# Optimization experiments

Measured on AMD Instinct MI355X. Metric: run time of the kernel, lower is better.

The kernel has to match this reference:

```python
import jax, jax.numpy as jnp
import numpy as np

B, CZ, E, V, H, W = 256, 512, 512, 4096, 16, 16  # batch, z_channels, embed_dim, vocab, latent HxW


def setup_inputs() -> dict:
    key = jax.random.key(0)
    k0, k1, k2, k3 = jax.random.split(key, 4)
    x = jax.random.normal(k0, (B, CZ, H, W), jnp.float32)          # encoder feature map
    pre_w = jax.random.normal(k1, (E, CZ), jnp.float32) * 0.02     # 1x1 pre_quant_conv weight
    pre_b = jnp.zeros((E,), jnp.float32)
    emb = jax.random.uniform(k2, (V, E), jnp.float32, -1.0 / V, 1.0 / V)  # codebook, uniform init as in module
    post_w = jax.random.normal(k3, (CZ, E), jnp.float32) * 0.02    # 1x1 post_quant_conv weight
    post_b = jnp.zeros((CZ,), jnp.float32)
    return dict(x=x, pre_w=pre_w, pre_b=pre_b, emb=emb, post_w=post_w, post_b=post_b)


def reference(x, pre_w, pre_b, emb, post_w, post_b):
    # pre_quant_conv: 1x1 Conv2d(CZ -> E)
    z = jnp.einsum('bchw,ec->behw', x, pre_w) + pre_b[None, :, None, None]
    b, e, h, w = z.shape
    # flatten spatial: (b h w, e)
    zf = z.transpose(0, 2, 3, 1).reshape(-1, e)
    # expanded squared-distance to codebook: ||z||^2 + ||c||^2 - 2 z.c
    dist = (jnp.sum(zf * zf, axis=1, keepdims=True)
            + jnp.sum(emb * emb, axis=1)
            - 2.0 * zf @ emb.T)                                    # [bhw, V]
    tokens = jnp.argmin(dist, axis=-1)                             # [bhw] int
    z_q = emb[tokens].reshape(b, h, w, e).transpose(0, 3, 1, 2)    # gather -> [b,e,h,w]
    # straight-through estimator
    dec_in = z + jax.lax.stop_gradient(z_q - z)
    # post_quant_conv: 1x1 Conv2d(E -> CZ)
    rec = jnp.einsum('behw,ce->bchw', dec_in, post_w) + post_b[None, :, None, None]
    return z, z_q, rec
```

## Files before the change

kernel.cpp:

```cpp
#include <hip/hip_runtime.h>
#include <hip/hip_bf16.h>

typedef unsigned short u16;
typedef unsigned int   u32;
typedef unsigned long long u64;

using short8 = __attribute__((ext_vector_type(8))) short;
using f32x4  = __attribute__((ext_vector_type(4))) float;
using u16x8  = __attribute__((ext_vector_type(8))) unsigned short;

#define AS_GLOBAL __attribute__((address_space(1)))
#define AS_LDS    __attribute__((address_space(3)))

__device__ __forceinline__ u16 f2b(float x){
  u32 u = __float_as_uint(x);
  u32 r = (u + 0x7FFFu + ((u >> 16) & 1u)) >> 16;
  return (u16)r;
}
__device__ __forceinline__ float b2f(u16 h){ return __uint_as_float(((u32)h) << 16); }

__device__ __forceinline__ void gload16(u16* l, const u16* g){
  __builtin_amdgcn_global_load_lds((const AS_GLOBAL u32*)g, (AS_LDS u32*)l, 16, 0, 0);
}

__device__ __forceinline__ u64 umin64(u64 a, u64 b){ return a < b ? a : b; }

__device__ __forceinline__ u64 shfl_xor_u64(u64 v, int m){
  u32 lo = __shfl_xor((u32)v, m, 64);
  u32 hi = __shfl_xor((u32)(v >> 32), m, 64);
  return ((u64)hi << 32) | lo;
}

__global__ void k_cvt(const float* __restrict__ w, u16* __restrict__ d, int n){
  int i = blockIdx.x * 256 + threadIdx.x;
  if (i < n) d[i] = f2b(w[i]);
}

__global__ void k_cnorm(const float* __restrict__ emb, float* __restrict__ cnorm){
  int v = blockIdx.x, lane = threadIdx.x;
  const float* r = emb + (size_t)v * 512;
  float s = 0.f;
  #pragma unroll
  for (int i = 0; i < 8; ++i){ float x = r[lane + i * 64]; s += x * x; }
  #pragma unroll
  for (int off = 32; off; off >>= 1) s += __shfl_down(s, off, 64);
  if (lane == 0) cnorm[v] = s;
}

__global__ void k_tcvt(const float* __restrict__ src, u16* __restrict__ d){
  __shared__ float t[64][65];
  const int bid = blockIdx.x;
  const int b  = bid >> 5;
  const int rb = (bid >> 2) & 7;
  const int cb = bid & 3;
  const float* s = src + ((size_t)b * 512 + (size_t)rb * 64) * 256 + cb * 64;
  const int tid = threadIdx.x;
  #pragma unroll
  for (int j = 0; j < 4; ++j){
    int fl = j * 256 + tid;
    int r = fl >> 4, c4 = (fl & 15) * 4;
    float4 v = *(const float4*)(s + (size_t)r * 256 + c4);
    t[r][c4 + 0] = v.x; t[r][c4 + 1] = v.y; t[r][c4 + 2] = v.z; t[r][c4 + 3] = v.w;
  }
  __syncthreads();
  u16* o = d + ((size_t)b * 256 + (size_t)cb * 64) * 512 + rb * 64;
  #pragma unroll
  for (int j = 0; j < 2; ++j){
    int fl = j * 256 + tid;
    int c = fl >> 3, r8 = (fl & 7) * 8;
    u16x8 hv;
    #pragma unroll
    for (int i = 0; i < 8; ++i) hv[i] = f2b(t[r8 + i][c]);
    *(u16x8*)(o + (size_t)c * 512 + r8) = hv;
  }
}

__global__ void k_zq(const u64* __restrict__ keys, const float* __restrict__ emb, float* __restrict__ zq){
  int sidx = blockIdx.x * 64 + threadIdx.x;
  int b = sidx >> 8, s = sidx & 255;
  int v = (int)(u32)keys[sidx];
  const float4* er = (const float4*)(emb + (size_t)v * 512);
  float* o = zq + (size_t)b * 512 * 256 + s;
  #pragma unroll 4
  for (int e4 = 0; e4 < 128; ++e4){
    float4 vv = er[e4];
    o[(size_t)(e4 * 4 + 0) * 256] = vv.x;
    o[(size_t)(e4 * 4 + 1) * 256] = vv.y;
    o[(size_t)(e4 * 4 + 2) * 256] = vv.z;
    o[(size_t)(e4 * 4 + 3) * 256] = vv.w;
  }
}

template<int MODE>
__global__ __launch_bounds__(256, 4) void k_gemm(
    const u16* __restrict__ Ah,
    const u16* __restrict__ Bh,
    const u64* __restrict__ gkeys,
    const float* __restrict__ bias,
    float* __restrict__ Cout,
    int M, int mtbits)
{
  constexpr int K = 512;
  __shared__ __align__(16) u16 sA[128 * 64];
  __shared__ __align__(16) u16 sB[128 * 64];

  const int tid  = threadIdx.x;
  const int lane = tid & 63;
  const int wid  = tid >> 6;
  const int wm = wid >> 1, wn = wid & 1;

  const int nwg = gridDim.x;
  const int chunk = nwg >> 3;
  const int pb = blockIdx.x;
  const int bid = (pb & 7) * chunk + (pb >> 3);

  const int mt = bid & ((1 << mtbits) - 1);
  const int nt = (bid >> mtbits) & 1;
  const int b  = bid >> (mtbits + 1);
  const int m0 = mt * 128;
  const int n0 = nt * 128;
  const int bbase = b * 256;

  const u16* ga[4];
  const u16* gb[4];
  int ldso[4];
  #pragma unroll
  for (int i = 0; i < 4; ++i){
    int e = i * 256 + tid;
    int r = e >> 3;
    int sl = (e & 7) ^ (r & 7);
    ldso[i] = e * 8;
    ga[i] = Ah + (size_t)(m0 + r) * K + sl * 8;
    size_t brow;
    if (MODE == 2) brow = (size_t)(u32)gkeys[bbase + n0 + r];
    else           brow = (size_t)(bbase + n0 + r);
    gb[i] = Bh + brow * K + sl * 8;
  }

  const f32x4 zero4 = {0.f, 0.f, 0.f, 0.f};
  f32x4 acc[4][4];
  #pragma unroll
  for (int i = 0; i < 4; ++i)
    #pragma unroll
    for (int j = 0; j < 4; ++j) acc[i][j] = zero4;

  int aoff[2][4], boff[2][4];
  #pragma unroll
  for (int ks = 0; ks < 2; ++ks)
    #pragma unroll
    for (int f = 0; f < 4; ++f){
      int rA = wm * 64 + f * 16 + (lane & 15);
      aoff[ks][f] = rA * 64 + (((ks * 4 + (lane >> 4)) ^ (rA & 7)) * 8);
      int rB = wn * 64 + f * 16 + (lane & 15);
      boff[ks][f] = rB * 64 + (((ks * 4 + (lane >> 4)) ^ (rB & 7)) * 8);
    }

  for (int kt = 0; kt < 8; ++kt){
    const int k0 = kt * 64;
    #pragma unroll
    for (int i = 0; i < 4; ++i){
      gload16(&sA[ldso[i]], ga[i] + k0);
      gload16(&sB[ldso[i]], gb[i] + k0);
    }
    __syncthreads();
    #pragma unroll
    for (int ks = 0; ks < 2; ++ks){
      short8 ah[4], bh[4];
      #pragma unroll
      for (int f = 0; f < 4; ++f){
        ah[f] = *(const short8*)&sA[aoff[ks][f]];
        bh[f] = *(const short8*)&sB[boff[ks][f]];
      }
      #pragma unroll
      for (int fm = 0; fm < 4; ++fm)
        #pragma unroll
        for (int fn = 0; fn < 4; ++fn)
          acc[fm][fn] = __builtin_amdgcn_mfma_f32_16x16x32_bf16(ah[fm], bh[fn], acc[fm][fn], 0, 0, 0);
    }
    __syncthreads();
  }

  const int row0 = m0 + wm * 64;
  const int col  = n0 + wn * 64 + (lane & 15);
  float* Cb = Cout + (size_t)b * M * 256;
  #pragma unroll
  for (int fm = 0; fm < 4; ++fm){
    #pragma unroll
    for (int j = 0; j < 4; ++j){
      int row = row0 + fm * 16 + (lane >> 4) * 4 + j;
      float bi = bias[row];
      #pragma unroll
      for (int fn = 0; fn < 4; ++fn)
        Cb[(size_t)row * 256 + col + fn * 16] = acc[fm][fn][j] + bi;
    }
  }
}

__global__ __launch_bounds__(512, 2) void k_gemm2(
    const u16* __restrict__ Ah,
    const u16* __restrict__ Bh,
    const float* __restrict__ cnorm,
    u64* __restrict__ okeys)
{
  __shared__ __align__(16) u16 lds[75776];

  const int tid  = threadIdx.x;
  const int lane = tid & 63;
  const int wid  = tid >> 6;
  const int wm   = wid >> 2;
  const int wn   = wid & 3;
  const int b    = blockIdx.x;
  const int bbase = b * 256;

  float* cn = (float*)&lds[65536];
  {
    const float4* c4 = (const float4*)cnorm;
    float4 a0 = c4[tid], a1 = c4[tid + 512];
    ((float4*)cn)[tid] = a0; ((float4*)cn)[tid + 512] = a1;
  }
  __syncthreads();

  const int l8 = lane >> 3;
  const int sl = (lane & 7) ^ l8;
  const int arb = (wid < 4) ? wid * 16 : 128 + (wid - 4) * 16;
  const int brb = (wid >> 1) * 64 + (wid & 1) * 16;
  const size_t aS = (size_t)(arb + l8) * 512 + sl * 8;
  const size_t bS = (size_t)(bbase + brb + l8) * 512 + sl * 8;
  const int dA = arb * 64 + lane * 8;
  const int dB = 16384 + brb * 64 + lane * 8;

#define STG_AFML(tp) if ((tp) < 128){ const u16* s_ = Ah + (size_t)((tp) >> 3) * 131072 + aS + ((tp) & 7) * 64; u16* d_ = &lds[((tp) & 1) * 32768 + dA]; gload16(d_, s_); gload16(d_ + 512, s_ + 4096); }
#define STG_AFMH(tp) if ((tp) < 128){ const u16* s_ = Ah + (size_t)((tp) >> 3) * 131072 + aS + 32768 + ((tp) & 7) * 64; u16* d_ = &lds[((tp) & 1) * 32768 + dA + 4096]; gload16(d_, s_); gload16(d_ + 512, s_ + 4096); }
#define STG_BFNL(tp) if ((tp) < 128){ const u16* s_ = Bh + bS + ((tp) & 7) * 64; u16* d_ = &lds[((tp) & 1) * 32768 + dB]; gload16(d_, s_); gload16(d_ + 512, s_ + 4096); }
#define STG_BFNH(tp) if ((tp) < 128){ const u16* s_ = Bh + bS + 16384 + ((tp) & 7) * 64; u16* d_ = &lds[((tp) & 1) * 32768 + dB + 2048]; gload16(d_, s_); gload16(d_ + 512, s_ + 4096); }

#define PH_WAIT(tau_) { if ((tau_) < 126){ asm volatile("s_waitcnt vmcnt(10)" ::: "memory"); } else { asm volatile("s_waitcnt vmcnt(0)" ::: "memory"); } \
  __builtin_amdgcn_s_barrier(); __builtin_amdgcn_sched_barrier(0); }

  int aoff[2][8], boff[2][4];
  #pragma unroll
  for (int ks = 0; ks < 2; ++ks){
    #pragma unroll
    for (int f = 0; f < 8; ++f){
      int rA = wm * 128 + f * 16 + (lane & 15);
      aoff[ks][f] = rA * 64 + (((ks * 4 + (lane >> 4)) ^ (rA & 7)) * 8);
    }
    #pragma unroll
    for (int f = 0; f < 4; ++f){
      int rB = wn * 64 + f * 16 + (lane & 15);
      boff[ks][f] = 16384 + rB * 64 + (((ks * 4 + (lane >> 4)) ^ (rB & 7)) * 8);
    }
  }

  const f32x4 zero4 = {0.f, 0.f, 0.f, 0.f};
  f32x4 acc[8][4];
  #pragma unroll
  for (int i = 0; i < 8; ++i)
    #pragma unroll
    for (int j = 0; j < 4; ++j) acc[i][j] = zero4;

  u64 best[4];
  #pragma unroll
  for (int i = 0; i < 4; ++i) best[i] = ~0ull;

  short8 ah[4][2], bhL[2][2], bhH[2][2];

  STG_AFML(0) STG_BFNL(0) STG_BFNH(0) STG_AFMH(0)
  STG_AFML(1) STG_BFNL(1) STG_BFNH(1)

  for (int mt = 0; mt < 16; ++mt){
    #pragma unroll 2
    for (int kt = 0; kt < 8; ++kt){
      const int tau = mt * 8 + kt;
      const int bb_ = (tau & 1) * 32768;

      PH_WAIT(tau);
      STG_AFMH(tau + 1)
      #pragma unroll
      for (int f = 0; f < 4; ++f){ ah[f][0] = *(const short8*)&lds[bb_ + aoff[0][f]]; ah[f][1] = *(const short8*)&lds[bb_ + aoff[1][f]]; }
      #pragma unroll
      for (int f = 0; f < 2; ++f){ bhL[f][0] = *(const short8*)&lds[bb_ + boff[0][f]]; bhL[f][1] = *(const short8*)&lds[bb_ + boff[1][f]]; }
      __builtin_amdgcn_s_setprio(1);
      #pragma unroll
      for (int fm = 0; fm < 4; ++fm)
        #pragma unroll
        for (int fn = 0; fn < 2; ++fn){
          acc[fm][fn] = __builtin_amdgcn_mfma_f32_16x16x32_bf16(ah[fm][0], bhL[fn][0], acc[fm][fn], 0, 0, 0);
          acc[fm][fn] = __builtin_amdgcn_mfma_f32_16x16x32_bf16(ah[fm][1], bhL[fn][1], acc[fm][fn], 0, 0, 0);
        }
      __builtin_amdgcn_s_setprio(0);
      __builtin_amdgcn_sched_barrier(0);

      PH_WAIT(tau);
      STG_AFML(tau + 2)
      #pragma unroll
      for (int f = 0; f < 2; ++f){ bhH[f][0] = *(const short8*)&lds[bb_ + boff[0][2 + f]]; bhH[f][1] = *(const short8*)&lds[bb_ + boff[1][2 + f]]; }
      __builtin_amdgcn_s_setprio(1);
      #pragma unroll
      for (int fm = 0; fm < 4; ++fm)
        #pragma unroll
        for (int fn = 0; fn < 2; ++fn){
          acc[fm][2 + fn] = __builtin_amdgcn_mfma_f32_16x16x32_bf16(ah[fm][0], bhH[fn][0], acc[fm][2 + fn], 0, 0, 0);
          acc[fm][2 + fn] = __builtin_amdgcn_mfma_f32_16x16x32_bf16(ah[fm][1], bhH[fn][1], acc[fm][2 + fn], 0, 0, 0);
        }
      __builtin_amdgcn_s_setprio(0);
      __builtin_amdgcn_sched_barrier(0);

      PH_WAIT(tau);
      STG_BFNL(tau + 2)
      #pragma unroll
      for (int f = 0; f < 4; ++f){ ah[f][0] = *(const short8*)&lds[bb_ + aoff[0][4 + f]]; ah[f][1] = *(const short8*)&lds[bb_ + aoff[1][4 + f]]; }
      __builtin_amdgcn_s_setprio(1);
      #pragma unroll
      for (int fm = 0; fm < 4; ++fm)
        #pragma unroll
        for (int fn = 0; fn < 2; ++fn){
          acc[4 + fm][2 + fn] = __builtin_amdgcn_mfma_f32_16x16x32_bf16(ah[fm][0], bhH[fn][0], acc[4 + fm][2 + fn], 0, 0, 0);
          acc[4 + fm][2 + fn] = __builtin_amdgcn_mfma_f32_16x16x32_bf16(ah[fm][1], bhH[fn][1], acc[4 + fm][2 + fn], 0, 0, 0);
        }
      __builtin_amdgcn_s_setprio(0);
      __builtin_amdgcn_sched_barrier(0);

      PH_WAIT(tau);
      STG_BFNH(tau + 2)
      __builtin_amdgcn_s_setprio(1);
      #pragma unroll
      for (int fm = 0; fm < 4; ++fm)
        #pragma unroll
        for (int fn = 0; fn < 2; ++fn){
          acc[4 + fm][fn] = __builtin_amdgcn_mfma_f32_16x16x32_bf16(ah[fm][0], bhL[fn][0], acc[4 + fm][fn], 0, 0, 0);
          acc[4 + fm][fn] = __builtin_amdgcn_mfma_f32_16x16x32_bf16(ah[fm][1], bhL[fn][1], acc[4 + fm][fn], 0, 0, 0);
        }
      __builtin_amdgcn_s_setprio(0);
      __builtin_amdgcn_sched_barrier(0);
    }

    #pragma unroll
    for (int fn = 0; fn < 4; ++fn){
      #pragma unroll
      for (int fm = 0; fm < 8; ++fm){
        #pragma unroll
        for (int j = 0; j < 4; ++j){
          int v = mt * 256 + wm * 128 + fm * 16 + (lane >> 4) * 4 + j;
          float sc = cn[v] - 2.0f * acc[fm][fn][j];
          u32 o = __float_as_uint(sc);
          o = (o & 0x80000000u) ? ~o : (o | 0x80000000u);
          best[fn] = umin64(best[fn], ((u64)o << 32) | (u32)v);
        }
      }
    }
    #pragma unroll
    for (int i = 0; i < 8; ++i)
      #pragma unroll
      for (int j = 0; j < 4; ++j) acc[i][j] = zero4;
  }

  #pragma unroll
  for (int fn = 0; fn < 4; ++fn){
    best[fn] = umin64(best[fn], shfl_xor_u64(best[fn], 16));
    best[fn] = umin64(best[fn], shfl_xor_u64(best[fn], 32));
  }
  u64* kbuf = (u64*)&lds[73728];
  __syncthreads();
  if (lane < 16){
    #pragma unroll
    for (int fn = 0; fn < 4; ++fn)
      kbuf[wm * 256 + wn * 64 + fn * 16 + lane] = best[fn];
  }
  __syncthreads();
  if (tid < 256)
    okeys[bbase + tid] = umin64(kbuf[tid], kbuf[256 + tid]);

#undef STG_AFML
#undef STG_AFMH
#undef STG_BFNL
#undef STG_BFNH
#undef PH_WAIT
}

extern "C" void kernel_launch(void* const* d_in, const int* in_sizes, int n_in,
                              void* d_out, int out_size, void* d_ws, size_t ws_size,
                              hipStream_t stream){
  const float* x      = (const float*)d_in[0];
  const float* pre_w  = (const float*)d_in[1];
  const float* pre_b  = (const float*)d_in[2];
  const float* emb    = (const float*)d_in[3];
  const float* post_w = (const float*)d_in[4];
  const float* post_b = (const float*)d_in[5];

  float* z_out   = (float*)d_out;
  float* zq_out  = z_out + 33554432;
  float* rec_out = z_out + 67108864;

  char* w = (char*)d_ws;
  u16* prew_b  = (u16*)(w);
  u16* postw_b = (u16*)(w + 524288);
  u16* emb_b   = (u16*)(w + 1048576);
  float* cnorm = (float*)(w + 5242880);
  u64* keys    = (u64*)(w + 5259264);
  u16* xb      = (u16*)(w + 5783552);
  u16* zb = xb;

  k_cvt  <<<1024, 256, 0, stream>>>(pre_w, prew_b, 262144);
  k_cvt  <<<1024, 256, 0, stream>>>(post_w, postw_b, 262144);
  k_cvt  <<<8192, 256, 0, stream>>>(emb, emb_b, 2097152);
  k_cnorm<<<4096, 64, 0, stream>>>(emb, cnorm);

  k_tcvt<<<8192, 256, 0, stream>>>(x, xb);

  k_gemm<0><<<256 * 2 * 4, 256, 0, stream>>>(prew_b, xb,
      nullptr, pre_b, z_out, 512, 2);

  k_tcvt<<<8192, 256, 0, stream>>>(z_out, zb);

  k_gemm2<<<256, 512, 0, stream>>>(emb_b, zb, cnorm, keys);

  k_zq<<<1024, 64, 0, stream>>>(keys, emb, zq_out);

  k_gemm<2><<<256 * 2 * 4, 256, 0, stream>>>(postw_b, emb_b,
      keys, post_b, rec_out, 512, 2);
}
```

Baseline: 546.8 us.

## Keep B operand fragments resident in registers and quad-buffer A tiles in LDS

The distance GEMM kernel now loads each wave's full K-extent of B (the flattened z tile) into registers once (bf[8][2][4], 64 short8 per lane). Only the codebook A tiles are streamed through LDS, using a 4-deep ring buffer with one barrier per k-step instead of four phases. This removes repeated LDS traffic and staging for B, and simplifies the pipeline. In exchange it greatly increases VGPR pressure, which is why launch bounds drop to one block per CU. That lowers occupancy and risks spilling.

```diff
diff --git a/kernel.cpp b/kernel.cpp
--- a/kernel.cpp
+++ b/kernel.cpp
@@ -196,7 +196,7 @@
   }
 }
 
-__global__ __launch_bounds__(512, 2) void k_gemm2(
+__global__ __launch_bounds__(512, 1) void k_gemm2(
     const u16* __restrict__ Ah,
     const u16* __restrict__ Bh,
     const float* __restrict__ cnorm,
@@ -215,42 +215,43 @@
   float* cn = (float*)&lds[65536];
   {
     const float4* c4 = (const float4*)cnorm;
-    float4 a0 = c4[tid], a1 = c4[tid + 512];
-    ((float4*)cn)[tid] = a0; ((float4*)cn)[tid + 512] = a1;
+    ((float4*)cn)[tid] = c4[tid];
+    ((float4*)cn)[tid + 512] = c4[tid + 512];
   }
   __syncthreads();
 
-  const int l8 = lane >> 3;
-  const int sl = (lane & 7) ^ l8;
-  const int arb = (wid < 4) ? wid * 16 : 128 + (wid - 4) * 16;
-  const int brb = (wid >> 1) * 64 + (wid & 1) * 16;
-  const size_t aS = (size_t)(arb + l8) * 512 + sl * 8;
-  const size_t bS = (size_t)(bbase + brb + l8) * 512 + sl * 8;
-  const int dA = arb * 64 + lane * 8;
-  const int dB = 16384 + brb * 64 + lane * 8;
-
-#define STG_AFML(tp) if ((tp) < 128){ const u16* s_ = Ah + (size_t)((tp) >> 3) * 131072 + aS + ((tp) & 7) * 64; u16* d_ = &lds[((tp) & 1) * 32768 + dA]; gload16(d_, s_); gload16(d_ + 512, s_ + 4096); }
-#define STG_AFMH(tp) if ((tp) < 128){ const u16* s_ = Ah + (size_t)((tp) >> 3) * 131072 + aS + 32768 + ((tp) & 7) * 64; u16* d_ = &lds[((tp) & 1) * 32768 + dA + 4096]; gload16(d_, s_); gload16(d_ + 512, s_ + 4096); }
-#define STG_BFNL(tp) if ((tp) < 128){ const u16* s_ = Bh + bS + ((tp) & 7) * 64; u16* d_ = &lds[((tp) & 1) * 32768 + dB]; gload16(d_, s_); gload16(d_ + 512, s_ + 4096); }
-#define STG_BFNH(tp) if ((tp) < 128){ const u16* s_ = Bh + bS + 16384 + ((tp) & 7) * 64; u16* d_ = &lds[((tp) & 1) * 32768 + dB + 2048]; gload16(d_, s_); gload16(d_ + 512, s_ + 4096); }
-
-#define PH_WAIT(tau_) { if ((tau_) < 126){ asm volatile("s_waitcnt vmcnt(10)" ::: "memory"); } else { asm volatile("s_waitcnt vmcnt(0)" ::: "memory"); } \
-  __builtin_amdgcn_s_barrier(); __builtin_amdgcn_sched_barrier(0); }
-
-  int aoff[2][8], boff[2][4];
-  #pragma unroll
-  for (int ks = 0; ks < 2; ++ks){
-    #pragma unroll
-    for (int f = 0; f < 8; ++f){
-      int rA = wm * 128 + f * 16 + (lane & 15);
-      aoff[ks][f] = rA * 64 + (((ks * 4 + (lane >> 4)) ^ (rA & 7)) * 8);
-    }
-    #pragma unroll
-    for (int f = 0; f < 4; ++f){
-      int rB = wn * 64 + f * 16 + (lane & 15);
-      boff[ks][f] = 16384 + rB * 64 + (((ks * 4 + (lane >> 4)) ^ (rB & 7)) * 8);
-    }
-  }
+  short8 bf[8][2][4];
+  {
+    const u16* bp = Bh + (size_t)(bbase + wn * 64 + (lane & 15)) * 512 + (lane >> 4) * 8;
+    #pragma unroll
+    for (int kt = 0; kt < 8; ++kt)
+      #pragma unroll
+      for (int ks = 0; ks < 2; ++ks)
+        #pragma unroll
+        for (int f = 0; f < 4; ++f)
+          bf[kt][ks][f] = *(const short8*)(bp + f * 8192 + kt * 64 + ks * 32);
+  }
+
+  const u16* ga[4];
+  #pragma unroll
+  for (int i = 0; i < 4; ++i){
+    int e = i * 512 + tid;
+    int r = e >> 3;
+    int sl = (e & 7) ^ (r & 7);
+    ga[i] = Ah + (size_t)r * 512 + sl * 8;
+  }
+  const int dofs = tid * 8;
+
+#define STG_A(bufc, off) { _Pragma("unroll") for (int i_ = 0; i_ < 4; ++i_) \
+    gload16(&lds[(bufc) * 16384 + i_ * 4096 + dofs], ga[i_] + (off)); }
+#define VM8 asm volatile("s_waitcnt vmcnt(8)" ::: "memory");
+#define VM4 asm volatile("s_waitcnt vmcnt(4)" ::: "memory");
+#define VM0 asm volatile("s_waitcnt vmcnt(0)" ::: "memory");
+
+  int aoffK[2];
+  #pragma unroll
+  for (int ks = 0; ks < 2; ++ks)
+    aoffK[ks] = (wm * 128 + (lane & 15)) * 64 + (((ks * 4 + (lane >> 4)) ^ (lane & 7)) * 8);
 
   const f32x4 zero4 = {0.f, 0.f, 0.f, 0.f};
   f32x4 acc[8][4];
@@ -263,76 +264,40 @@
   #pragma unroll
   for (int i = 0; i < 4; ++i) best[i] = ~0ull;
 
-  short8 ah[4][2], bhL[2][2], bhH[2][2];
-
-  STG_AFML(0) STG_BFNL(0) STG_BFNH(0) STG_AFMH(0)
-  STG_AFML(1) STG_BFNL(1) STG_BFNH(1)
+  STG_A(0, 0)
+  STG_A(1, 64)
 
   for (int mt = 0; mt < 16; ++mt){
-    #pragma unroll 2
+    const size_t amt = (size_t)mt * 131072;
+
+    #pragma unroll
     for (int kt = 0; kt < 8; ++kt){
-      const int tau = mt * 8 + kt;
-      const int bb_ = (tau & 1) * 32768;
-
-      PH_WAIT(tau);
-      STG_AFMH(tau + 1)
-      #pragma unroll
-      for (int f = 0; f < 4; ++f){ ah[f][0] = *(const short8*)&lds[bb_ + aoff[0][f]]; ah[f][1] = *(const short8*)&lds[bb_ + aoff[1][f]]; }
-      #pragma unroll
-      for (int f = 0; f < 2; ++f){ bhL[f][0] = *(const short8*)&lds[bb_ + boff[0][f]]; bhL[f][1] = *(const short8*)&lds[bb_ + boff[1][f]]; }
-      __builtin_amdgcn_s_setprio(1);
-      #pragma unroll
-      for (int fm = 0; fm < 4; ++fm)
-        #pragma unroll
-        for (int fn = 0; fn < 2; ++fn){
-          acc[fm][fn] = __builtin_amdgcn_mfma_f32_16x16x32_bf16(ah[fm][0], bhL[fn][0], acc[fm][fn], 0, 0, 0);
-          acc[fm][fn] = __builtin_amdgcn_mfma_f32_16x16x32_bf16(ah[fm][1], bhL[fn][1], acc[fm][fn], 0, 0, 0);
-        }
-      __builtin_amdgcn_s_setprio(0);
+      if (kt < 6){
+        STG_A((kt + 2) & 3, amt + (kt + 2) * 64)
+      } else {
+        if (mt < 15) STG_A((kt + 2) & 3, amt + 131072 + (kt - 6) * 64)
+      }
+      if (kt < 6){ VM8 }
+      else if (kt == 6){ if (mt < 15){ VM8 } else { VM4 } }
+      else          { if (mt < 15){ VM8 } else { VM0 } }
+      __builtin_amdgcn_s_barrier();
       __builtin_amdgcn_sched_barrier(0);
 
-      PH_WAIT(tau);
-      STG_AFML(tau + 2)
-      #pragma unroll
-      for (int f = 0; f < 2; ++f){ bhH[f][0] = *(const short8*)&lds[bb_ + boff[0][2 + f]]; bhH[f][1] = *(const short8*)&lds[bb_ + boff[1][2 + f]]; }
-      __builtin_amdgcn_s_setprio(1);
-      #pragma unroll
-      for (int fm = 0; fm < 4; ++fm)
-        #pragma unroll
-        for (int fn = 0; fn < 2; ++fn){
-          acc[fm][2 + fn] = __builtin_amdgcn_mfma_f32_16x16x32_bf16(ah[fm][0], bhH[fn][0], acc[fm][2 + fn], 0, 0, 0);
-          acc[fm][2 + fn] = __builtin_amdgcn_mfma_f32_16x16x32_bf16(ah[fm][1], bhH[fn][1], acc[fm][2 + fn], 0, 0, 0);
-        }
-      __builtin_amdgcn_s_setprio(0);
-      __builtin_amdgcn_sched_barrier(0);
-
-      PH_WAIT(tau);
-      STG_BFNL(tau + 2)
-      #pragma unroll
-      for (int f = 0; f < 4; ++f){ ah[f][0] = *(const short8*)&lds[bb_ + aoff[0][4 + f]]; ah[f][1] = *(const short8*)&lds[bb_ + aoff[1][4 + f]]; }
-      __builtin_amdgcn_s_setprio(1);
-      #pragma unroll
-      for (int fm = 0; fm < 4; ++fm)
-        #pragma unroll
-        for (int fn = 0; fn < 2; ++fn){
-          acc[4 + fm][2 + fn] = __builtin_amdgcn_mfma_f32_16x16x32_bf16(ah[fm][0], bhH[fn][0], acc[4 + fm][2 + fn], 0, 0, 0);
-          acc[4 + fm][2 + fn] = __builtin_amdgcn_mfma_f32_16x16x32_bf16(ah[fm][1], bhH[fn][1], acc[4 + fm][2 + fn], 0, 0, 0);
-        }
-      __builtin_amdgcn_s_setprio(0);
-      __builtin_amdgcn_sched_barrier(0);
-
-      PH_WAIT(tau);
-      STG_BFNH(tau + 2)
-      __builtin_amdgcn_s_setprio(1);
-      #pragma unroll
-      for (int fm = 0; fm < 4; ++fm)
-        #pragma unroll
-        for (int fn = 0; fn < 2; ++fn){
-          acc[4 + fm][fn] = __builtin_amdgcn_mfma_f32_16x16x32_bf16(ah[fm][0], bhL[fn][0], acc[4 + fm][fn], 0, 0, 0);
-          acc[4 + fm][fn] = __builtin_amdgcn_mfma_f32_16x16x32_bf16(ah[fm][1], bhL[fn][1], acc[4 + fm][fn], 0, 0, 0);
-        }
-      __builtin_amdgcn_s_setprio(0);
-      __builtin_amdgcn_sched_barrier(0);
+      const int rbuf = (kt & 3) * 16384;
+      #pragma unroll
+      for (int ks = 0; ks < 2; ++ks){
+        short8 ah[8];
+        #pragma unroll
+        for (int f = 0; f < 8; ++f)
+          ah[f] = *(const short8*)&lds[rbuf + aoffK[ks] + f * 1024];
+        __builtin_amdgcn_s_setprio(1);
+        #pragma unroll
+        for (int fm = 0; fm < 8; ++fm)
+          #pragma unroll
+          for (int f = 0; f < 4; ++f)
+            acc[fm][f] = __builtin_amdgcn_mfma_f32_16x16x32_bf16(ah[fm], bf[kt][ks][f], acc[fm][f], 0, 0, 0);
+        __builtin_amdgcn_s_setprio(0);
+      }
     }
 
     #pragma unroll
@@ -371,11 +336,10 @@
   if (tid < 256)
     okeys[bbase + tid] = umin64(kbuf[tid], kbuf[256 + tid]);
 
-#undef STG_AFML
-#undef STG_AFMH
-#undef STG_BFNL
-#undef STG_BFNH
-#undef PH_WAIT
+#undef STG_A
+#undef VM8
+#undef VM4
+#undef VM0
 }
 
 extern "C" void kernel_launch(void* const* d_in, const int* in_sizes, int n_in,
```

New measurement: 741.3 us. +35.6%, slower.
